# Kernel optimization log

Measured on AMD Instinct MI355X. Metric: run time of the kernel, lower is better.

The kernel has to match this reference:

```python
import jax, jax.numpy as jnp
import numpy as np

N, T, V, CIN, COUT = 64, 12, 256, 64, 64


def _conv1x1(h, w, b):
    # h: [n,c,v,w], w: [o,c] (1x1 conv kernel squeezed), b: [o]
    return jnp.einsum('ncvw,oc->novw', h, w) + b[None, :, None, None]


def setup_inputs() -> dict:
    key = jax.random.key(0)
    ks = jax.random.split(key, 8)
    x = jax.random.normal(ks[0], (N, CIN, T, V), jnp.float32)
    feats = jax.random.normal(ks[1], (N, 7, V, V), jnp.float32)
    mask = (jax.random.uniform(ks[2], (N, 1, V, V)) < 0.3).astype(jnp.float32)
    A = jnp.concatenate([feats, mask], axis=1)  # [N, 8, V, V]
    init = lambda k, shape, fan: jax.random.normal(k, shape, jnp.float32) / np.sqrt(fan).astype(np.float32)
    conv_w = init(ks[3], (COUT, CIN), CIN)
    conv_b = jnp.zeros((COUT,), jnp.float32)
    w1 = init(ks[4], (16, 7), 7)
    b1 = jnp.zeros((16,), jnp.float32)
    w2 = init(ks[5], (32, 16), 16)
    b2 = jnp.zeros((32,), jnp.float32)
    w3 = init(ks[6], (64, 32), 32)
    b3 = jnp.zeros((64,), jnp.float32)
    return dict(x=x, A=A, conv_w=conv_w, conv_b=conv_b,
                w1=w1, b1=b1, w2=w2, b2=b2, w3=w3, b3=b3)


def reference(x, A, conv_w, conv_b, w1, b1, w2, b2, w3, b3):
    # 1x1 temporal conv on node features: [n,cin,t,v] -> [n,cout,t,v]
    x = jnp.einsum('nctv,oc->notv', x, conv_w) + conv_b[None, :, None, None]
    mask = A[:, 7:]          # [n,1,v,v]
    h = A[:, :7]             # [n,7,v,v]
    # adjmatder MLP (dropout is identity at inference)
    h = jax.nn.relu(_conv1x1(h, w1, b1))
    h = jax.nn.relu(_conv1x1(h, w2, b2))
    h = jax.nn.relu(_conv1x1(h, w3, b3))   # [n,64,v,v]
    Aw = h * mask
    # per-channel graph convolution: [n,c,t,v] x [n,c,v,w] -> [n,c,t,w]
    out = jnp.einsum('nctv,ncvw->nctw', x, Aw)
    return out, Aw
```

## Files before the change

### kernel.cpp

```cpp
#include <hip/hip_runtime.h>
#include <hip/hip_bf16.h>

#define NB   64
#define TT   12
#define VV   256
#define CIN  64
#define COUT 64
#define VSQ  65536

typedef float f32x4 __attribute__((ext_vector_type(4)));
using s16x8 = __attribute__((ext_vector_type(8))) short;

__device__ __forceinline__ unsigned short f2bf(float f) {
    union { __hip_bfloat16 h; unsigned short u; } cv;
    cv.h = __float2bfloat16(f);
    return cv.u;
}

__global__ __launch_bounds__(256) void k1_conv(
    const float* __restrict__ x, const float* __restrict__ w,
    const float* __restrict__ b, float* __restrict__ y)
{
    const int nt = blockIdx.x;
    const int n  = nt / TT;
    const int t  = nt % TT;
    const int v  = threadIdx.x;

    const float* xp = x + ((long)n * CIN * TT + t) * VV + v;
    float xv[CIN];
    #pragma unroll 8
    for (int c = 0; c < CIN; ++c)
        xv[c] = xp[(long)c * TT * VV];

    float* yp = y + ((long)n * COUT * TT + t) * VV + v;

    for (int o0 = 0; o0 < COUT; o0 += 16) {
        float acc[16];
        #pragma unroll
        for (int i = 0; i < 16; ++i) acc[i] = b[o0 + i];
        #pragma unroll 8
        for (int c = 0; c < CIN; ++c) {
            const float xc = xv[c];
            #pragma unroll
            for (int i = 0; i < 16; ++i)
                acc[i] += w[(o0 + i) * CIN + c] * xc;
        }
        #pragma unroll
        for (int i = 0; i < 16; ++i)
            yp[(long)(o0 + i) * TT * VV] = acc[i];
    }
}

__global__ __launch_bounds__(256) void k2_mlp(
    const float* __restrict__ A,
    const float* __restrict__ w1, const float* __restrict__ b1,
    const float* __restrict__ w2, const float* __restrict__ b2,
    const float* __restrict__ w3, const float* __restrict__ b3,
    float* __restrict__ Aw)
{
    __shared__ unsigned int afrag[16 * 256];
    __shared__ float ms[256];

    const int  tid  = threadIdx.x;
    const long gpos = (long)blockIdx.x * 256;
    const int  n    = (int)(gpos >> 16);
    const int  rem0 = (int)(gpos & (VSQ - 1));

    {
        const float* ap = A + ((long)n * 8 << 16) + rem0 + tid;
        float f[7];
        #pragma unroll
        for (int c = 0; c < 7; ++c) f[c] = ap[(long)c << 16];
        ms[tid] = ap[(long)7 << 16];

        float h1[16];
        #pragma unroll
        for (int o = 0; o < 16; ++o) {
            float s = b1[o];
            #pragma unroll
            for (int k = 0; k < 7; ++k) s += w1[o * 7 + k] * f[k];
            h1[o] = fmaxf(s, 0.f);
        }
        float h2[32];
        #pragma unroll
        for (int o = 0; o < 32; ++o) {
            float s = b2[o];
            #pragma unroll
            for (int k = 0; k < 16; ++k) s += w2[o * 16 + k] * h1[k];
            h2[o] = fmaxf(s, 0.f);
        }

        const int m = tid >> 4;
        const int r = tid & 15;
        #pragma unroll
        for (int kk = 0; kk < 16; ++kk) {
            const unsigned int pr = (unsigned int)f2bf(h2[2 * kk])
                                  | ((unsigned int)f2bf(h2[2 * kk + 1]) << 16);
            afrag[m * 256 + (kk >> 2) * 64 + r * 4 + (kk & 3)] = pr;
        }
    }
    __syncthreads();

    const int lane = tid & 63;
    const int wave = tid >> 6;
    const int lc   = lane & 15;
    const int lq   = lane >> 4;

    s16x8 bfr[4];
    float bias[4];
    #pragma unroll
    for (int ntile = 0; ntile < 4; ++ntile) {
        const int c = ntile * 16 + lc;
        const float* wr = w3 + c * 32 + lq * 8;
        s16x8 bf;
        #pragma unroll
        for (int i = 0; i < 8; ++i) bf[i] = (short)f2bf(wr[i]);
        bfr[ntile]  = bf;
        bias[ntile] = b3[c];
    }

    float* awbase = Aw + ((long)n * COUT << 16) + rem0;

    #pragma unroll
    for (int j = 0; j < 4; ++j) {
        const int mt = wave * 4 + j;
        const s16x8 afr = *reinterpret_cast<const s16x8*>(&afrag[mt * 256 + lane * 4]);
        const int pbase = mt * 16 + lq * 4;
        const f32x4 mv = *reinterpret_cast<const f32x4*>(&ms[pbase]);
        #pragma unroll
        for (int ntile = 0; ntile < 4; ++ntile) {
            f32x4 acc = (f32x4)(bias[ntile]);
            acc = __builtin_amdgcn_mfma_f32_16x16x32_bf16(afr, bfr[ntile], acc, 0, 0, 0);
            f32x4 r;
            #pragma unroll
            for (int u = 0; u < 4; ++u) r[u] = fmaxf(acc[u], 0.f) * mv[u];
            __builtin_nontemporal_store(r, reinterpret_cast<f32x4*>(
                awbase + ((long)(ntile * 16 + lc) << 16) + pbase));
        }
    }
}

__global__ __launch_bounds__(256) void k3_einsum(
    const float* __restrict__ Aw, const float* __restrict__ y,
    float* __restrict__ out)
{
    __shared__ float ys[4][TT][VV];

    const int n   = blockIdx.x >> 4;
    const int c0  = (blockIdx.x & 15) * 4;
    const int tid = threadIdx.x;
    const int cq  = tid >> 6;
    const int w4  = (tid & 63) * 4;

    {
        const float* src = y + ((long)(n * COUT + c0) * TT) * VV;
        float* dst = &ys[0][0][0];
        #pragma unroll
        for (int it = 0; it < 12; ++it) {
            const int idx = tid + it * 256;
            *reinterpret_cast<float4*>(dst + idx * 4) =
                *reinterpret_cast<const float4*>(src + idx * 4);
        }
    }
    __syncthreads();

    const float* awp = Aw + (((long)(n * COUT + c0 + cq)) << 16) + w4;
    float4 acc[TT];
    #pragma unroll
    for (int t = 0; t < TT; ++t) acc[t] = make_float4(0.f, 0.f, 0.f, 0.f);

    for (int v0 = 0; v0 < VV; v0 += 4) {
        float4 xs[TT];
        #pragma unroll
        for (int t = 0; t < TT; ++t)
            xs[t] = *reinterpret_cast<const float4*>(&ys[cq][t][v0]);

        const f32x4 aw0 = __builtin_nontemporal_load(
            reinterpret_cast<const f32x4*>(awp + (long)(v0 + 0) * VV));
        const f32x4 aw1 = __builtin_nontemporal_load(
            reinterpret_cast<const f32x4*>(awp + (long)(v0 + 1) * VV));
        const f32x4 aw2 = __builtin_nontemporal_load(
            reinterpret_cast<const f32x4*>(awp + (long)(v0 + 2) * VV));
        const f32x4 aw3 = __builtin_nontemporal_load(
            reinterpret_cast<const f32x4*>(awp + (long)(v0 + 3) * VV));

        #pragma unroll
        for (int t = 0; t < TT; ++t) {
            acc[t].x += xs[t].x * aw0.x + xs[t].y * aw1.x + xs[t].z * aw2.x + xs[t].w * aw3.x;
            acc[t].y += xs[t].x * aw0.y + xs[t].y * aw1.y + xs[t].z * aw2.y + xs[t].w * aw3.y;
            acc[t].z += xs[t].x * aw0.z + xs[t].y * aw1.z + xs[t].z * aw2.z + xs[t].w * aw3.z;
            acc[t].w += xs[t].x * aw0.w + xs[t].y * aw1.w + xs[t].z * aw2.w + xs[t].w * aw3.w;
        }
    }

    float* op = out + ((long)(n * COUT + c0 + cq) * TT) * VV + w4;
    #pragma unroll
    for (int t = 0; t < TT; ++t)
        *reinterpret_cast<float4*>(op + t * VV) = acc[t];
}

extern "C" void kernel_launch(void* const* d_in, const int* in_sizes, int n_in,
                              void* d_out, int out_size, void* d_ws, size_t ws_size,
                              hipStream_t stream)
{
    const float* x      = (const float*)d_in[0];
    const float* A      = (const float*)d_in[1];
    const float* conv_w = (const float*)d_in[2];
    const float* conv_b = (const float*)d_in[3];
    const float* w1     = (const float*)d_in[4];
    const float* b1     = (const float*)d_in[5];
    const float* w2     = (const float*)d_in[6];
    const float* b2     = (const float*)d_in[7];
    const float* w3     = (const float*)d_in[8];
    const float* b3     = (const float*)d_in[9];

    float* out = (float*)d_out;
    float* Aw  = (float*)d_out + (long)NB * COUT * TT * VV;
    const size_t y_bytes = (size_t)NB * COUT * TT * VV * sizeof(float);

    float* y = (ws_size >= y_bytes) ? (float*)d_ws : out;

    k1_conv<<<NB * TT, 256, 0, stream>>>(x, conv_w, conv_b, y);

    k2_mlp<<<(NB * VSQ) / 256, 256, 0, stream>>>(A, w1, b1, w2, b2, w3, b3, Aw);

    k3_einsum<<<NB * (COUT / 4), 256, 0, stream>>>(Aw, y, out);
}
```

Measured before the change: 638.8 us.

## Fuse adjacency MLP and graph einsum into one kernel over column tiles

Adds a kernel that computes the MLP-weighted adjacency for a 16-column tile in chunks of 16 rows, writes those values to the Aw output, then reads them back (likely from cache) and accumulates the graph convolution for all 64 channels in the same block. It replaces the separate MLP and einsum kernels when workspace is available, so the full Aw tensor no longer has to be re-read from HBM in a second pass. The cost is two barriers per chunk, y being read straight from global memory without LDS staging, and a grid of only 1024 blocks that each loop serially over all 256 rows.

After: 836.1 us. 30.9% more time.

```diff
diff --git a/kernel.cpp b/kernel.cpp
--- a/kernel.cpp
+++ b/kernel.cpp
@@ -7,6 +7,8 @@
 #define CIN  64
 #define COUT 64
 #define VSQ  65536
+#define WT   16
+#define VC   16
 
 typedef float f32x4 __attribute__((ext_vector_type(4)));
 using s16x8 = __attribute__((ext_vector_type(8))) short;
@@ -49,6 +51,126 @@
         for (int i = 0; i < 16; ++i)
             yp[(long)(o0 + i) * TT * VV] = acc[i];
     }
+}
+
+__global__ __launch_bounds__(256) void k23_fused(
+    const float* __restrict__ A,
+    const float* __restrict__ w1, const float* __restrict__ b1,
+    const float* __restrict__ w2, const float* __restrict__ b2,
+    const float* __restrict__ w3, const float* __restrict__ b3,
+    const float* __restrict__ y,
+    float* __restrict__ Aw, float* __restrict__ out)
+{
+    __shared__ unsigned int afrag[16 * 256];
+    __shared__ float ms[256];
+
+    const int n   = blockIdx.x & 63;
+    const int w0  = (blockIdx.x >> 6) * WT;
+    const int tid = threadIdx.x;
+
+    const int vj   = tid >> 4;
+    const int wj   = tid & 15;
+    const int lane = tid & 63;
+    const int wave = tid >> 6;
+    const int lc   = lane & 15;
+    const int lq   = lane >> 4;
+    const int cb   = tid >> 2;
+    const int wg   = tid & 3;
+
+    s16x8 bfr[4];
+    float bias[4];
+    #pragma unroll
+    for (int ntile = 0; ntile < 4; ++ntile) {
+        const int c = ntile * 16 + lc;
+        const float* wr = w3 + c * 32 + lq * 8;
+        s16x8 bf;
+        #pragma unroll
+        for (int i = 0; i < 8; ++i) bf[i] = (short)f2bf(wr[i]);
+        bfr[ntile]  = bf;
+        bias[ntile] = b3[c];
+    }
+
+    f32x4 acc[TT];
+    #pragma unroll
+    for (int t = 0; t < TT; ++t) acc[t] = (f32x4)(0.f);
+
+    const float* Abase = A + ((long)n * 8 << 16);
+    float*       awn   = Aw + ((long)n * COUT << 16);
+    const float* ybase = y + (long)(n * COUT + cb) * TT * VV;
+    const float* awrd  = Aw + (((long)(n * COUT + cb)) << 16) + w0 + wg * 4;
+
+    for (int v0 = 0; v0 < VV; v0 += VC) {
+        {
+            const int pos = (v0 + vj) * VV + (w0 + wj);
+            const float* ap = Abase + pos;
+            float f[7];
+            #pragma unroll
+            for (int c = 0; c < 7; ++c) f[c] = ap[(long)c << 16];
+            ms[tid] = ap[(long)7 << 16];
+
+            float h1[16];
+            #pragma unroll
+            for (int o = 0; o < 16; ++o) {
+                float s = b1[o];
+                #pragma unroll
+                for (int k = 0; k < 7; ++k) s += w1[o * 7 + k] * f[k];
+                h1[o] = fmaxf(s, 0.f);
+            }
+            float h2[32];
+            #pragma unroll
+            for (int o = 0; o < 32; ++o) {
+                float s = b2[o];
+                #pragma unroll
+                for (int k = 0; k < 16; ++k) s += w2[o * 16 + k] * h1[k];
+                h2[o] = fmaxf(s, 0.f);
+            }
+            #pragma unroll
+            for (int kk = 0; kk < 16; ++kk) {
+                const unsigned int pr = (unsigned int)f2bf(h2[2 * kk])
+                                      | ((unsigned int)f2bf(h2[2 * kk + 1]) << 16);
+                afrag[vj * 256 + (kk >> 2) * 64 + wj * 4 + (kk & 3)] = pr;
+            }
+        }
+        __syncthreads();
+
+        #pragma unroll
+        for (int j = 0; j < 4; ++j) {
+            const int mt = wave * 4 + j;
+            const s16x8 afr = *reinterpret_cast<const s16x8*>(&afrag[mt * 256 + lane * 4]);
+            const int prow  = mt * 16 + lq * 4;
+            const f32x4 mv  = *reinterpret_cast<const f32x4*>(&ms[prow]);
+            const long  vrow = (long)(v0 + mt) * VV + w0 + lq * 4;
+            #pragma unroll
+            for (int ntile = 0; ntile < 4; ++ntile) {
+                f32x4 a = (f32x4)(bias[ntile]);
+                a = __builtin_amdgcn_mfma_f32_16x16x32_bf16(afr, bfr[ntile], a, 0, 0, 0);
+                f32x4 r;
+                #pragma unroll
+                for (int u = 0; u < 4; ++u) r[u] = fmaxf(a[u], 0.f) * mv[u];
+                *reinterpret_cast<f32x4*>(awn + ((long)(ntile * 16 + lc) << 16) + vrow) = r;
+            }
+        }
+        __syncthreads();
+
+        f32x4 awv[VC];
+        #pragma unroll
+        for (int vv = 0; vv < VC; ++vv)
+            awv[vv] = *reinterpret_cast<const f32x4*>(awrd + (long)(v0 + vv) * VV);
+        #pragma unroll
+        for (int t = 0; t < TT; ++t) {
+            #pragma unroll
+            for (int q = 0; q < 4; ++q) {
+                const f32x4 yv = *reinterpret_cast<const f32x4*>(ybase + t * VV + v0 + q * 4);
+                acc[t] += yv.x * awv[q * 4 + 0] + yv.y * awv[q * 4 + 1]
+                        + yv.z * awv[q * 4 + 2] + yv.w * awv[q * 4 + 3];
+            }
+        }
+    }
+
+    float* obase = out + (long)(n * COUT + cb) * TT * VV + w0 + wg * 4;
+    #pragma unroll
+    for (int t = 0; t < TT; ++t)
+        __builtin_nontemporal_store(acc[t], reinterpret_cast<f32x4*>(obase + t * VV));
 }
 
 __global__ __launch_bounds__(256) void k2_mlp(
@@ -89,7 +211,6 @@
             for (int k = 0; k < 16; ++k) s += w2[o * 16 + k] * h1[k];
             h2[o] = fmaxf(s, 0.f);
         }
-
         const int m = tid >> 4;
         const int r = tid & 15;
         #pragma unroll
@@ -129,11 +250,11 @@
         const f32x4 mv = *reinterpret_cast<const f32x4*>(&ms[pbase]);
         #pragma unroll
         for (int ntile = 0; ntile < 4; ++ntile) {
-            f32x4 acc = (f32x4)(bias[ntile]);
-            acc = __builtin_amdgcn_mfma_f32_16x16x32_bf16(afr, bfr[ntile], acc, 0, 0, 0);
+            f32x4 a = (f32x4)(bias[ntile]);
+            a = __builtin_amdgcn_mfma_f32_16x16x32_bf16(afr, bfr[ntile], a, 0, 0, 0);
             f32x4 r;
             #pragma unroll
-            for (int u = 0; u < 4; ++u) r[u] = fmaxf(acc[u], 0.f) * mv[u];
+            for (int u = 0; u < 4; ++u) r[u] = fmaxf(a[u], 0.f) * mv[u];
             __builtin_nontemporal_store(r, reinterpret_cast<f32x4*>(
                 awbase + ((long)(ntile * 16 + lc) << 16) + pbase));
         }
@@ -218,11 +339,14 @@
     float* Aw  = (float*)d_out + (long)NB * COUT * TT * VV;
     const size_t y_bytes = (size_t)NB * COUT * TT * VV * sizeof(float);
 
-    float* y = (ws_size >= y_bytes) ? (float*)d_ws : out;
-
-    k1_conv<<<NB * TT, 256, 0, stream>>>(x, conv_w, conv_b, y);
-
-    k2_mlp<<<(NB * VSQ) / 256, 256, 0, stream>>>(A, w1, b1, w2, b2, w3, b3, Aw);
-
-    k3_einsum<<<NB * (COUT / 4), 256, 0, stream>>>(Aw, y, out);
-}
+    if (ws_size >= y_bytes) {
+        float* y = (float*)d_ws;
+        k1_conv<<<NB * TT, 256, 0, stream>>>(x, conv_w, conv_b, y);
+        k23_fused<<<NB * (VV / WT), 256, 0, stream>>>(
+            A, w1, b1, w2, b2, w3, b3, y, Aw, out);
+    } else {
+        k1_conv<<<NB * TT, 256, 0, stream>>>(x, conv_w, conv_b, out);
+        k2_mlp<<<(NB * VSQ) / 256, 256, 0, stream>>>(A, w1, b1, w2, b2, w3, b3, Aw);
+        k3_einsum<<<NB * (COUT / 4), 256, 0, stream>>>(Aw, out, out);
+    }
+}
```
